# Kernel optimization log

Hardware: AMD Instinct MI355X
Metric: run time of the kernel (lower is better)

Reference implementation:

```python
import jax, jax.numpy as jnp
import numpy as np

HIDDEN = 1024
HEADS = 16
HEAD_DIM = HIDDEN // HEADS
EPS = 1e-5


def _layernorm(x, w, b):
    mu = jnp.mean(x, axis=-1, keepdims=True)
    var = jnp.mean(jnp.square(x - mu), axis=-1, keepdims=True)
    return (x - mu) * jax.lax.rsqrt(var + EPS) * w + b


def setup_inputs() -> dict:
    key = jax.random.key(0)
    ks = jax.random.split(key, 8)
    D = HIDDEN
    x = jax.random.normal(ks[0], (4, 4096, D), dtype=jnp.float32)
    s = 0.02
    return {
        "x": x,
        "qkv_w": jax.random.normal(ks[1], (3 * D, D), jnp.float32) * s,
        "qkv_b": jnp.zeros((3 * D,), jnp.float32),
        "proj_w": jax.random.normal(ks[2], (D, D), jnp.float32) * s,
        "proj_b": jnp.zeros((D,), jnp.float32),
        "ln1_w": jnp.ones((D,), jnp.float32),
        "ln1_b": jnp.zeros((D,), jnp.float32),
        "ln2_w": jnp.ones((D,), jnp.float32),
        "ln2_b": jnp.zeros((D,), jnp.float32),
        "mlp_w1": jax.random.normal(ks[3], (4 * D, D), jnp.float32) * s,
        "mlp_b1": jnp.zeros((4 * D,), jnp.float32),
        "mlp_w2": jax.random.normal(ks[4], (D, 4 * D), jnp.float32) * s,
        "mlp_b2": jnp.zeros((D,), jnp.float32),
    }


def reference(x, qkv_w, qkv_b, proj_w, proj_b, ln1_w, ln1_b, ln2_w, ln2_b,
              mlp_w1, mlp_b1, mlp_w2, mlp_b2):
    B, L, D = x.shape
    h = _layernorm(x, ln1_w, ln1_b)
    qkv = (h @ qkv_w.T + qkv_b).reshape(B, L, 3, HEADS, HEAD_DIM)
    q, k, v = qkv[:, :, 0], qkv[:, :, 1], qkv[:, :, 2]  # (B, L, H, hd)
    # NOTE: faithful to source - NO (L,H) transpose, so attention mixes
    # across the head axis per token: scores shape (B, L, H, H).
    attn = jnp.einsum('blhd,blgd->blhg', q, k) / np.sqrt(HEAD_DIM).astype(np.float32)
    attn = jax.nn.softmax(attn, axis=-1)
    out = jnp.einsum('blhg,blgd->blhd', attn, v).reshape(B, L, D)
    out = out @ proj_w.T + proj_b
    x = x + out
    h2 = _layernorm(x, ln2_w, ln2_b)
    mlp = jax.nn.gelu(h2 @ mlp_w1.T + mlp_b1, approximate=False) @ mlp_w2.T + mlp_b2
    return x + mlp
```

## Files before the change

### kernel.cpp

```cpp
#include <hip/hip_runtime.h>
#include <cstdint>
#include <cmath>


#define NTOK   16384
#define DMODEL 1024

typedef __bf16 bf16x8 __attribute__((ext_vector_type(8)));
typedef float  f32x4  __attribute__((ext_vector_type(4)));
typedef unsigned int __attribute__((address_space(1))) as1_uint;
typedef unsigned int __attribute__((address_space(3))) as3_uint;

__device__ __forceinline__ unsigned short f2bf(float f) {
    unsigned int u = __builtin_bit_cast(unsigned int, f);
    u += 0x7fffu + ((u >> 16) & 1u);
    return (unsigned short)(u >> 16);
}
__device__ __forceinline__ float bf2f(unsigned short s) {
    unsigned int u = ((unsigned int)s) << 16;
    return __builtin_bit_cast(float, u);
}

__device__ __forceinline__ void g2l16(const unsigned short* g, unsigned short* l) {
    __builtin_amdgcn_global_load_lds((const as1_uint*)g, (as3_uint*)l, 16, 0, 0);
}

__device__ __forceinline__ f32x4 mfma16(bf16x8 a, bf16x8 b, f32x4 c) {
    return __builtin_amdgcn_mfma_f32_16x16x32_bf16(a, b, c, 0, 0, 0);
}

__global__ __launch_bounds__(256) void cast_f32_bf16(
    const float4* __restrict__ in, ushort4* __restrict__ out, int n4) {
    int i = blockIdx.x * 256 + threadIdx.x;
    if (i < n4) {
        float4 v = in[i];
        ushort4 o;
        o.x = f2bf(v.x); o.y = f2bf(v.y); o.z = f2bf(v.z); o.w = f2bf(v.w);
        out[i] = o;
    }
}

__global__ __launch_bounds__(256) void ln_cast(
    const float* __restrict__ x, const float* __restrict__ w,
    const float* __restrict__ b, unsigned short* __restrict__ out) {
    int tok = blockIdx.x;
    int t   = threadIdx.x;
    float4 v = ((const float4*)x)[tok * 256 + t];
    float s  = v.x + v.y + v.z + v.w;
    float ss = v.x * v.x + v.y * v.y + v.z * v.z + v.w * v.w;
    #pragma unroll
    for (int off = 32; off > 0; off >>= 1) {
        s  += __shfl_down(s, off);
        ss += __shfl_down(ss, off);
    }
    __shared__ float red[8];
    int wave = t >> 6;
    if ((t & 63) == 0) { red[wave * 2] = s; red[wave * 2 + 1] = ss; }
    __syncthreads();
    s  = red[0] + red[2] + red[4] + red[6];
    ss = red[1] + red[3] + red[5] + red[7];
    float mu  = s * (1.0f / 1024.0f);
    float var = ss * (1.0f / 1024.0f) - mu * mu;
    float rs  = rsqrtf(var + 1e-5f);
    float4 wv = ((const float4*)w)[t];
    float4 bv = ((const float4*)b)[t];
    ushort4 o;
    o.x = f2bf((v.x - mu) * rs * wv.x + bv.x);
    o.y = f2bf((v.y - mu) * rs * wv.y + bv.y);
    o.z = f2bf((v.z - mu) * rs * wv.z + bv.z);
    o.w = f2bf((v.w - mu) * rs * wv.w + bv.w);
    ((ushort4*)out)[tok * 256 + t] = o;
}

__global__ __launch_bounds__(256) void attn_heads(
    const unsigned short* __restrict__ qkv, unsigned short* __restrict__ out) {
    __shared__ float sQ[1024], sK[1024], sV[1024];
    __shared__ float sS[256];
    int tok = blockIdx.x;
    int t   = threadIdx.x;
    const unsigned short* base = qkv + (size_t)tok * 3072;
    for (int i = t; i < 1024; i += 256) {
        sQ[i] = bf2f(base[i]);
        sK[i] = bf2f(base[1024 + i]);
        sV[i] = bf2f(base[2048 + i]);
    }
    __syncthreads();
    {
        int h = t >> 4, g = t & 15;
        float s = 0.0f;
        #pragma unroll
        for (int d = 0; d < 64; ++d) s += sQ[h * 64 + d] * sK[g * 64 + d];
        sS[h * 16 + g] = s * 0.125f;
    }
    __syncthreads();
    if (t < 16) {
        float mx = -1e30f;
        for (int g = 0; g < 16; ++g) mx = fmaxf(mx, sS[t * 16 + g]);
        float sum = 0.0f;
        for (int g = 0; g < 16; ++g) {
            float e = expf(sS[t * 16 + g] - mx);
            sS[t * 16 + g] = e;
            sum += e;
        }
        float inv = 1.0f / sum;
        for (int g = 0; g < 16; ++g) sS[t * 16 + g] *= inv;
    }
    __syncthreads();
    #pragma unroll
    for (int j = 0; j < 4; ++j) {
        int o = t + 256 * j;
        int h = o >> 6, d = o & 63;
        float s = 0.0f;
        #pragma unroll
        for (int g = 0; g < 16; ++g) s += sS[h * 16 + g] * sV[g * 64 + d];
        out[(size_t)tok * 1024 + o] = f2bf(s);
    }
}

#define BM 256
#define BN 256

#define READ_A(kh) { _Pragma("unroll")                                        \
    for (int mf = 0; mf < 8; ++mf)                                            \
        a[mf] = *(const bf16x8*)(lA + bo + (kh)*8192 + pA + mf*512 + roA); }
#define READ_B(kh, i0, i1) {                                                  \
    b[i0] = *(const bf16x8*)(lB + bo + (kh)*8192 + pB + (i0)*512 + roB);      \
    b[i1] = *(const bf16x8*)(lB + bo + (kh)*8192 + pB + (i1)*512 + roB); }
#define MFMA_BLK(i0, i1) {                                                    \
    __builtin_amdgcn_s_setprio(1);                                            \
    _Pragma("unroll")                                                         \
    for (int mf = 0; mf < 8; ++mf) {                                          \
        acc[mf][i0] = mfma16(a[mf], b[i0], acc[mf][i0]);                      \
        acc[mf][i1] = mfma16(a[mf], b[i1], acc[mf][i1]);                      \
    }                                                                         \
    __builtin_amdgcn_s_setprio(0); }

template <int EPI>
__global__ __launch_bounds__(512, 2) void gemm_bf16(
    const unsigned short* __restrict__ A, const unsigned short* __restrict__ W,
    const float* __restrict__ bias, const float* resid, void* Cout,
    int M, int N, int K) {
    __shared__ __align__(16) unsigned short sA[2][4][4096];
    __shared__ __align__(16) unsigned short sB[2][4][4096];
    unsigned short* const lA = &sA[0][0][0];
    unsigned short* const lB = &sB[0][0][0];

    const int t    = threadIdx.x;
    const int lane = t & 63;
    const int w    = t >> 6;
    const int wm   = w >> 2;
    const int wn   = w & 3;

    const int gm = M >> 8, gn = N >> 8;
    const int nwg = gm * gn;
    int m0, n0;
    if (((gm & 7) == 0) && ((gn & 3) == 0) && ((nwg & 255) == 0)) {
        const int xcd = blockIdx.x & 7;
        const int j   = blockIdx.x >> 3;
        const int pos = j & 31;
        const int spx = nwg >> 8;
        const int sid = xcd * spx + (j >> 5);
        const int sgm = gm >> 3;
        m0 = ((sid % sgm) * 8 + (pos >> 2)) << 8;
        n0 = ((sid / sgm) * 4 + (pos & 3)) << 8;
    } else {
        m0 = (blockIdx.x / gn) << 8;
        n0 = (blockIdx.x % gn) << 8;
    }

    const int srow = w * 16 + (lane >> 2);
    const int cg8  = ((lane & 3) ^ ((lane >> 3) & 3)) * 8;
    const unsigned short* gA0 = A + (size_t)(m0 +       srow) * K + cg8;
    const unsigned short* gA1 = A + (size_t)(m0 + 128 + srow) * K + cg8;
    const unsigned short* gB0 = W + (size_t)(n0 +       srow) * K + cg8;
    const unsigned short* gB1 = W + (size_t)(n0 + 128 + srow) * K + cg8;
    const int wst = w * 512;

    const int fr   = lane & 15, fq = lane >> 4;
    const int csw8 = (fq ^ ((fr >> 1) & 3)) * 8;
    const int roA  = fr * 32 + csw8;
    const int roB  = (wn & 1) * 2048 + fr * 32 + csw8;
    const int pA   = wm * 4096;
    const int pB   = (wn >> 1) * 4096;

    f32x4 acc[8][4] = {};

    g2l16(gA0,      lA + 0 * 4096 + wst);
    g2l16(gA1,      lA + 1 * 4096 + wst);
    g2l16(gB0,      lB + 0 * 4096 + wst);
    g2l16(gB1,      lB + 1 * 4096 + wst);
    g2l16(gA0 + 32, lA + 2 * 4096 + wst);
    g2l16(gA1 + 32, lA + 3 * 4096 + wst);
    g2l16(gB0 + 32, lB + 2 * 4096 + wst);
    g2l16(gB1 + 32, lB + 3 * 4096 + wst);
    asm volatile("s_waitcnt vmcnt(4)" ::: "memory");
    __builtin_amdgcn_s_barrier();

    const int NT = K >> 6;
    for (int kt = 0; kt < NT - 1; ++kt) {
        const int bo = (kt & 1) << 14;
        const int so = bo ^ 16384;
        const size_t kg = (size_t)kt * 64 + 64;
        bf16x8 a[8], b[4];

        READ_A(0); READ_B(0, 0, 1);
        g2l16(gA0 + kg, lA + so + wst);
        g2l16(gA1 + kg, lA + so + 4096 + wst);
        MFMA_BLK(0, 1);
        __builtin_amdgcn_s_barrier();
        READ_B(0, 2, 3);
        g2l16(gB0 + kg, lB + so + wst);
        g2l16(gB1 + kg, lB + so + 4096 + wst);
        MFMA_BLK(2, 3);
        asm volatile("s_waitcnt vmcnt(4)" ::: "memory");
        __builtin_amdgcn_s_barrier();
        READ_A(1); READ_B(1, 0, 1);
        g2l16(gA0 + kg + 32, lA + so + 8192 + wst);
        g2l16(gA1 + kg + 32, lA + so + 8192 + 4096 + wst);
        MFMA_BLK(0, 1);
        __builtin_amdgcn_s_barrier();
        READ_B(1, 2, 3);
        g2l16(gB0 + kg + 32, lB + so + 8192 + wst);
        g2l16(gB1 + kg + 32, lB + so + 8192 + 4096 + wst);
        MFMA_BLK(2, 3);
        asm volatile("s_waitcnt vmcnt(4)" ::: "memory");
        __builtin_amdgcn_s_barrier();
    }

    {
        const int bo = ((NT - 1) & 1) << 14;
        bf16x8 a[8], b[4];
        READ_A(0); READ_B(0, 0, 1);
        MFMA_BLK(0, 1);
        __builtin_amdgcn_s_barrier();
        READ_B(0, 2, 3);
        MFMA_BLK(2, 3);
        asm volatile("s_waitcnt vmcnt(0)" ::: "memory");
        __builtin_amdgcn_s_barrier();
        READ_A(1); READ_B(1, 0, 1);
        MFMA_BLK(0, 1);
        READ_B(1, 2, 3);
        MFMA_BLK(2, 3);
    }

    float bv[4];
    #pragma unroll
    for (int nf = 0; nf < 4; ++nf) bv[nf] = bias[n0 + wn * 64 + nf * 16 + fr];
    #pragma unroll
    for (int mf = 0; mf < 8; ++mf) {
        #pragma unroll
        for (int e = 0; e < 4; ++e) {
            const int row = m0 + wm * 128 + mf * 16 + fq * 4 + e;
            const size_t rbase = (size_t)row * N + n0 + wn * 64 + fr;
            #pragma unroll
            for (int nf = 0; nf < 4; ++nf) {
                const size_t idx = rbase + nf * 16;
                float v = acc[mf][nf][e] + bv[nf];
                if (EPI == 0) {
                    ((unsigned short*)Cout)[idx] = f2bf(v);
                } else if (EPI == 1) {
                    ((float*)Cout)[idx] = v + resid[idx];
                } else {
                    float s  = 0.7978845608f * (v + 0.044715f * v * v * v);
                    float e2 = __expf(2.0f * s);
                    float th = 1.0f - 2.0f / (e2 + 1.0f);
                    ((unsigned short*)Cout)[idx] = f2bf(0.5f * v * (1.0f + th));
                }
            }
        }
    }
}

#undef READ_A
#undef READ_B
#undef MFMA_BLK

extern "C" void kernel_launch(void* const* d_in, const int* in_sizes, int n_in,
                              void* d_out, int out_size, void* d_ws, size_t ws_size,
                              hipStream_t stream) {
    const float* x      = (const float*)d_in[0];
    const float* qkv_w  = (const float*)d_in[1];
    const float* qkv_b  = (const float*)d_in[2];
    const float* proj_w = (const float*)d_in[3];
    const float* proj_b = (const float*)d_in[4];
    const float* ln1_w  = (const float*)d_in[5];
    const float* ln1_b  = (const float*)d_in[6];
    const float* ln2_w  = (const float*)d_in[7];
    const float* ln2_b  = (const float*)d_in[8];
    const float* mlp_w1 = (const float*)d_in[9];
    const float* mlp_b1 = (const float*)d_in[10];
    const float* mlp_w2 = (const float*)d_in[11];
    const float* mlp_b2 = (const float*)d_in[12];
    float* out = (float*)d_out;

    const size_t WB = 25165824;
    char* ws = (char*)d_ws;
    unsigned short* w_qkv  = (unsigned short*)(ws);
    unsigned short* w_proj = (unsigned short*)(ws + 6291456);
    unsigned short* w_m1   = (unsigned short*)(ws + 8388608);
    unsigned short* w_m2   = (unsigned short*)(ws + 16777216);

    int T = NTOK;
    while (T >= 256 && WB + (size_t)T * 12288 > ws_size) T >>= 1;
    if (T < 256) {
        hipMemcpyAsync(out, x, (size_t)NTOK * DMODEL * sizeof(float),
                       hipMemcpyDeviceToDevice, stream);
        return;
    }

    unsigned short* hbuf = (unsigned short*)(ws + WB);
    unsigned short* abuf = (unsigned short*)(ws + WB + (size_t)T * 2048);
    unsigned short* qmbuf= (unsigned short*)(ws + WB + (size_t)T * 4096);

    cast_f32_bf16<<<3072, 256, 0, stream>>>((const float4*)qkv_w,  (ushort4*)w_qkv,  786432);
    cast_f32_bf16<<<1024, 256, 0, stream>>>((const float4*)proj_w, (ushort4*)w_proj, 262144);
    cast_f32_bf16<<<4096, 256, 0, stream>>>((const float4*)mlp_w1, (ushort4*)w_m1,   1048576);
    cast_f32_bf16<<<4096, 256, 0, stream>>>((const float4*)mlp_w2, (ushort4*)w_m2,   1048576);

    for (int tok0 = 0; tok0 < NTOK; tok0 += T) {
        const float* xc   = x   + (size_t)tok0 * DMODEL;
        float*       outc = out + (size_t)tok0 * DMODEL;
        const int my = T / BM;

        ln_cast<<<T, 256, 0, stream>>>(xc, ln1_w, ln1_b, hbuf);
        gemm_bf16<0><<<(3072 / BN) * my, 512, 0, stream>>>(
            hbuf, w_qkv, qkv_b, nullptr, qmbuf, T, 3072, 1024);
        attn_heads<<<T, 256, 0, stream>>>(qmbuf, abuf);
        gemm_bf16<1><<<(1024 / BN) * my, 512, 0, stream>>>(
            abuf, w_proj, proj_b, xc, (void*)outc, T, 1024, 1024);
        ln_cast<<<T, 256, 0, stream>>>(outc, ln2_w, ln2_b, hbuf);
        gemm_bf16<2><<<(4096 / BN) * my, 512, 0, stream>>>(
            hbuf, w_m1, mlp_b1, nullptr, qmbuf, T, 4096, 1024);
        gemm_bf16<1><<<(1024 / BN) * my, 512, 0, stream>>>(
            qmbuf, w_m2, mlp_b2, outc, (void*)outc, T, 1024, 4096);
    }
}
```

Before: 857.9 us.

## Restructure GEMM main loop into quadrant-based ping-pong schedule with staggered A/B prefetch

Rewrites the bf16 GEMM inner loop so each wave computes its 128x64 tile in four 64x32 quadrants, loading A and B fragments for both k-halves at once. Global-to-LDS prefetches of A and B for later k-steps are interleaved between the quadrants, with B prefetched two steps ahead, and explicit barriers and lgkmcnt waits gate each phase. The aim is finer-grained overlap of LDS reads, global loads and MFMA work, in the style of the HipKittens 8-wave schedule. The cost is many more barriers per iteration, and clamped redundant loads on the last iteration.

```diff
diff --git a/kernel.cpp b/kernel.cpp
--- a/kernel.cpp
+++ b/kernel.cpp
@@ -120,20 +120,33 @@
 #define BM 256
 #define BN 256
 
-#define READ_A(kh) { _Pragma("unroll")                                        \
-    for (int mf = 0; mf < 8; ++mf)                                            \
-        a[mf] = *(const bf16x8*)(lA + bo + (kh)*8192 + pA + mf*512 + roA); }
-#define READ_B(kh, i0, i1) {                                                  \
-    b[i0] = *(const bf16x8*)(lB + bo + (kh)*8192 + pB + (i0)*512 + roB);      \
-    b[i1] = *(const bf16x8*)(lB + bo + (kh)*8192 + pB + (i1)*512 + roB); }
-#define MFMA_BLK(i0, i1) {                                                    \
+#define DS_A(bufo, h) { _Pragma("unroll")                                     \
+    for (int mf = 0; mf < 4; ++mf) {                                          \
+        a[mf][0] = *(const bf16x8*)(lA + (bufo) + 0*8192 + pA +               \
+                                    ((h)*4+mf)*512 + roA);                    \
+        a[mf][1] = *(const bf16x8*)(lA + (bufo) + 1*8192 + pA +               \
+                                    ((h)*4+mf)*512 + roA); } }
+#define DS_B(bufo, np, dst) { _Pragma("unroll")                               \
+    for (int nf = 0; nf < 2; ++nf) {                                          \
+        dst[nf][0] = *(const bf16x8*)(lB + (bufo) + 0*8192 + pB +             \
+                                      ((np)*2+nf)*512 + roB);                 \
+        dst[nf][1] = *(const bf16x8*)(lB + (bufo) + 1*8192 + pB +             \
+                                      ((np)*2+nf)*512 + roB); } }
+#define MFMA_Q(h, np, bb) {                                                   \
     __builtin_amdgcn_s_setprio(1);                                            \
     _Pragma("unroll")                                                         \
-    for (int mf = 0; mf < 8; ++mf) {                                          \
-        acc[mf][i0] = mfma16(a[mf], b[i0], acc[mf][i0]);                      \
-        acc[mf][i1] = mfma16(a[mf], b[i1], acc[mf][i1]);                      \
-    }                                                                         \
+    for (int kh = 0; kh < 2; ++kh)                                            \
+      _Pragma("unroll")                                                       \
+      for (int mf = 0; mf < 4; ++mf)                                          \
+        _Pragma("unroll")                                                     \
+        for (int nf = 0; nf < 2; ++nf)                                        \
+          acc[(h)*4+mf][(np)*2+nf] =                                          \
+              mfma16(a[mf][kh], bb[nf][kh], acc[(h)*4+mf][(np)*2+nf]);        \
     __builtin_amdgcn_s_setprio(0); }
+#define BARR  __builtin_amdgcn_s_barrier()
+#define LGKM0 asm volatile("s_waitcnt lgkmcnt(0)" ::: "memory")
+#define LGKM8 asm volatile("s_waitcnt lgkmcnt(8)" ::: "memory")
+#define VM4   asm volatile("s_waitcnt vmcnt(4)" ::: "memory")
 
 template <int EPI>
 __global__ __launch_bounds__(512, 2) void gemm_bf16(
@@ -183,65 +196,76 @@
     const int pA   = wm * 4096;
     const int pB   = (wn >> 1) * 4096;
 
-    f32x4 acc[8][4] = {};
-
+    f32x4  acc[8][4] = {};
+    bf16x8 a[4][2], bL[2][2], bH[2][2];
+
+    g2l16(gB0,      lB + 0 * 4096 + wst);
+    g2l16(gB1,      lB + 1 * 4096 + wst);
+    g2l16(gB0 + 32, lB + 2 * 4096 + wst);
+    g2l16(gB1 + 32, lB + 3 * 4096 + wst);
     g2l16(gA0,      lA + 0 * 4096 + wst);
     g2l16(gA1,      lA + 1 * 4096 + wst);
-    g2l16(gB0,      lB + 0 * 4096 + wst);
-    g2l16(gB1,      lB + 1 * 4096 + wst);
     g2l16(gA0 + 32, lA + 2 * 4096 + wst);
     g2l16(gA1 + 32, lA + 3 * 4096 + wst);
-    g2l16(gB0 + 32, lB + 2 * 4096 + wst);
-    g2l16(gB1 + 32, lB + 3 * 4096 + wst);
-    asm volatile("s_waitcnt vmcnt(4)" ::: "memory");
-    __builtin_amdgcn_s_barrier();
-
-    const int NT = K >> 6;
-    for (int kt = 0; kt < NT - 1; ++kt) {
-        const int bo = (kt & 1) << 14;
-        const int so = bo ^ 16384;
-        const size_t kg = (size_t)kt * 64 + 64;
-        bf16x8 a[8], b[4];
-
-        READ_A(0); READ_B(0, 0, 1);
-        g2l16(gA0 + kg, lA + so + wst);
-        g2l16(gA1 + kg, lA + so + 4096 + wst);
-        MFMA_BLK(0, 1);
-        __builtin_amdgcn_s_barrier();
-        READ_B(0, 2, 3);
-        g2l16(gB0 + kg, lB + so + wst);
-        g2l16(gB1 + kg, lB + so + 4096 + wst);
-        MFMA_BLK(2, 3);
-        asm volatile("s_waitcnt vmcnt(4)" ::: "memory");
-        __builtin_amdgcn_s_barrier();
-        READ_A(1); READ_B(1, 0, 1);
-        g2l16(gA0 + kg + 32, lA + so + 8192 + wst);
-        g2l16(gA1 + kg + 32, lA + so + 8192 + 4096 + wst);
-        MFMA_BLK(0, 1);
-        __builtin_amdgcn_s_barrier();
-        READ_B(1, 2, 3);
-        g2l16(gB0 + kg + 32, lB + so + 8192 + wst);
-        g2l16(gB1 + kg + 32, lB + so + 8192 + 4096 + wst);
-        MFMA_BLK(2, 3);
-        asm volatile("s_waitcnt vmcnt(4)" ::: "memory");
-        __builtin_amdgcn_s_barrier();
-    }
-
-    {
-        const int bo = ((NT - 1) & 1) << 14;
-        bf16x8 a[8], b[4];
-        READ_A(0); READ_B(0, 0, 1);
-        MFMA_BLK(0, 1);
-        __builtin_amdgcn_s_barrier();
-        READ_B(0, 2, 3);
-        MFMA_BLK(2, 3);
-        asm volatile("s_waitcnt vmcnt(0)" ::: "memory");
-        __builtin_amdgcn_s_barrier();
-        READ_A(1); READ_B(1, 0, 1);
-        MFMA_BLK(0, 1);
-        READ_B(1, 2, 3);
-        MFMA_BLK(2, 3);
-    }
+    g2l16(gB0 + 64, lB + 16384 + 0 * 4096 + wst);
+    g2l16(gB1 + 64, lB + 16384 + 1 * 4096 + wst);
+    g2l16(gB0 + 96, lB + 16384 + 2 * 4096 + wst);
+    g2l16(gB1 + 96, lB + 16384 + 3 * 4096 + wst);
+    VM4;
+    BARR;
+
+    const int NITER = K >> 7;
+    for (int i = 0; i < NITER; ++i) {
+        const size_t kA1 = (size_t)(2 * i + 1) * 64;
+        size_t k0 = (size_t)(2 * i + 2) * 64;
+        if (k0 > (size_t)(K - 64)) k0 = (size_t)(K - 64);
+        size_t k1 = (size_t)(2 * i + 3) * 64;
+        if (k1 > (size_t)(K - 64)) k1 = (size_t)(K - 64);
+
+        DS_A(0, 0); DS_B(0, 0, bL);
+        g2l16(gA0 + kA1, lA + 16384 + 0 * 4096 + wst);
+        g2l16(gA1 + kA1, lA + 16384 + 1 * 4096 + wst);
+        LGKM8; BARR; LGKM0;
+        MFMA_Q(0, 0, bL); BARR;
+        DS_B(0, 1, bH);
+        g2l16(gA0 + kA1 + 32, lA + 16384 + 2 * 4096 + wst);
+        g2l16(gA1 + kA1 + 32, lA + 16384 + 3 * 4096 + wst);
+        BARR; LGKM0;
+        MFMA_Q(0, 1, bH); BARR;
+        DS_A(0, 1);
+        g2l16(gB0 + k0, lB + 0 * 4096 + wst);
+        g2l16(gB1 + k0, lB + 1 * 4096 + wst);
+        BARR; LGKM0;
+        MFMA_Q(1, 1, bH); BARR;
+        g2l16(gB0 + k0 + 32, lB + 2 * 4096 + wst);
+        g2l16(gB1 + k0 + 32, lB + 3 * 4096 + wst);
+        BARR;
+        MFMA_Q(1, 0, bL);
+        VM4;
+        BARR;
+        DS_A(16384, 0); DS_B(16384, 0, bL);
+        g2l16(gA0 + k0, lA + 0 * 4096 + wst);
+        g2l16(gA1 + k0, lA + 1 * 4096 + wst);
+        LGKM8; BARR; LGKM0;
+        MFMA_Q(0, 0, bL); BARR;
+        DS_B(16384, 1, bH);
+        g2l16(gA0 + k0 + 32, lA + 2 * 4096 + wst);
+        g2l16(gA1 + k0 + 32, lA + 3 * 4096 + wst);
+        BARR; LGKM0;
+        MFMA_Q(0, 1, bH); BARR;
+        DS_A(16384, 1);
+        g2l16(gB0 + k1, lB + 16384 + 0 * 4096 + wst);
+        g2l16(gB1 + k1, lB + 16384 + 1 * 4096 + wst);
+        BARR; LGKM0;
+        MFMA_Q(1, 1, bH); BARR;
+        g2l16(gB0 + k1 + 32, lB + 16384 + 2 * 4096 + wst);
+        g2l16(gB1 + k1 + 32, lB + 16384 + 3 * 4096 + wst);
+        BARR;
+        MFMA_Q(1, 0, bL);
+        VM4;
+        BARR;
+    }
+    asm volatile("s_waitcnt vmcnt(0)" ::: "memory");
 
     float bv[4];
     #pragma unroll
@@ -271,9 +295,13 @@
     }
 }
 
-#undef READ_A
-#undef READ_B
-#undef MFMA_BLK
+#undef DS_A
+#undef DS_B
+#undef MFMA_Q
+#undef BARR
+#undef LGKM0
+#undef LGKM8
+#undef VM4
 
 extern "C" void kernel_launch(void* const* d_in, const int* in_sizes, int n_in,
                               void* d_out, int out_size, void* d_ws, size_t ws_size,
```

Result: slower. 877.8 us (+2.3%).
